# Kernel optimization log

Hardware: AMD Instinct MI355X
Metric: run time of the kernel (lower is better)

## Reference

```python
import jax, jax.numpy as jnp
import numpy as np

NUM_CUSTOMERS = 300000
NUM_PRODUCTS = 150000
NUM_GROUPS = 2000
NUM_BRANDS = 500
EMB_DIM = 64
NUM_LAYERS = 3


def setup_inputs() -> dict:
    key = jax.random.key(0)
    ks = jax.random.split(key, 20)
    def ri(k, n, hi):
        return jax.random.randint(k, (n,), 0, hi, dtype=jnp.int32)
    return {
        'cust_w': 0.1 * jax.random.normal(ks[0], (NUM_CUSTOMERS, EMB_DIM), jnp.float32),
        'prod_w': 0.1 * jax.random.normal(ks[1], (NUM_PRODUCTS, EMB_DIM), jnp.float32),
        'group_w': 0.1 * jax.random.normal(ks[2], (NUM_GROUPS, EMB_DIM), jnp.float32),
        'brand_w': 0.1 * jax.random.normal(ks[3], (NUM_BRANDS, EMB_DIM), jnp.float32),
        'purch_src': ri(ks[4], 2000000, NUM_CUSTOMERS),
        'purch_dst': ri(ks[5], 2000000, NUM_PRODUCTS),
        'pby_src': ri(ks[6], 2000000, NUM_PRODUCTS),
        'pby_dst': ri(ks[7], 2000000, NUM_CUSTOMERS),
        'sim_src': ri(ks[8], 500000, NUM_PRODUCTS),
        'sim_dst': ri(ks[9], 500000, NUM_PRODUCTS),
        'cop_src': ri(ks[10], 1000000, NUM_PRODUCTS),
        'cop_dst': ri(ks[11], 1000000, NUM_PRODUCTS),
        'bel_src': ri(ks[12], 150000, NUM_PRODUCTS),
        'bel_dst': ri(ks[13], 150000, NUM_GROUPS),
        'comp_src': ri(ks[14], 300000, NUM_PRODUCTS),
        'comp_dst': ri(ks[15], 300000, NUM_BRANDS),
    }


def _propagate(src_idx, tgt_idx, tgt_emb, n_src):
    # gather target embeddings along edges, scatter-add into source buckets,
    # normalize by source out-degree (clamped to >= 1) -- LightGCN mean-agg.
    msg = tgt_emb[tgt_idx]                                    # [E, D]
    agg = jax.ops.segment_sum(msg, src_idx, num_segments=n_src)
    cnt = jax.ops.segment_sum(jnp.ones(src_idx.shape, tgt_emb.dtype),
                              src_idx, num_segments=n_src)
    return agg / jnp.maximum(cnt, 1.0)[:, None]


def reference(cust_w, prod_w, group_w, brand_w,
              purch_src, purch_dst, pby_src, pby_dst,
              sim_src, sim_dst, cop_src, cop_dst,
              bel_src, bel_dst, comp_src, comp_dst):
    customer_emb, product_emb = cust_w, prod_w
    group_emb, brand_emb = group_w, brand_w
    customer_embs = [customer_emb]
    product_embs = [product_emb]
    for _ in range(NUM_LAYERS):
        customer_to_product = _propagate(purch_src, purch_dst, product_emb, NUM_CUSTOMERS)
        product_agg = product_emb
        product_agg = product_agg + _propagate(pby_src, pby_dst, customer_emb, NUM_PRODUCTS)
        product_agg = product_agg + 0.5 * _propagate(sim_src, sim_dst, product_emb, NUM_PRODUCTS)
        product_agg = product_agg + 0.3 * _propagate(cop_src, cop_dst, product_emb, NUM_PRODUCTS)
        product_agg = product_agg + 0.2 * _propagate(bel_src, bel_dst, group_emb, NUM_PRODUCTS)
        product_agg = product_agg + 0.2 * _propagate(comp_src, comp_dst, brand_emb, NUM_PRODUCTS)
        customer_emb = customer_to_product
        product_emb = product_agg
        customer_embs.append(customer_emb)
        product_embs.append(product_emb)
    final_customer = jnp.mean(jnp.stack(customer_embs, 0), axis=0)
    final_product = jnp.mean(jnp.stack(product_embs, 0), axis=0)
    # group/brand embeddings are never updated -> mean of identical copies
    return (final_customer, final_product, group_emb, brand_emb)
```

## Files before the change

### kernel.cpp

```cpp
#include <hip/hip_runtime.h>

#define NC 300000
#define NP 150000
#define NG 2000
#define NB 500
#define SCAN_B 1024
#define BK_SHIFT 11
#define BK_KEYS 2048
#define NBKT 513
#define CH 8192
#define ROWS (NP + NC)
#define RCH 4096

typedef unsigned int u32;
typedef float  f32x4 __attribute__((ext_vector_type(4)));
typedef unsigned int u32x4 __attribute__((ext_vector_type(4)));

static inline unsigned cdiv(long long a, long long b) { return (unsigned)((a + b - 1) / b); }

__device__ __forceinline__ float b2f(u32 h) {
    union { u32 u; float f; } c; c.u = h << 16; return c.f;
}
__device__ __forceinline__ u32 f2b(float f) {
    union { float f; u32 u; } c; c.f = f;
    return (c.u + 0x7FFFu + ((c.u >> 16) & 1u)) >> 16;
}
__device__ __forceinline__ void unpack8(uint4 v, float* o) {
    o[0] = b2f(v.x & 0xFFFFu); o[1] = b2f(v.x >> 16);
    o[2] = b2f(v.y & 0xFFFFu); o[3] = b2f(v.y >> 16);
    o[4] = b2f(v.z & 0xFFFFu); o[5] = b2f(v.z >> 16);
    o[6] = b2f(v.w & 0xFFFFu); o[7] = b2f(v.w >> 16);
}
__device__ __forceinline__ void unpack8v(u32x4 v, float* o) {
    o[0] = b2f(v.x & 0xFFFFu); o[1] = b2f(v.x >> 16);
    o[2] = b2f(v.y & 0xFFFFu); o[3] = b2f(v.y >> 16);
    o[4] = b2f(v.z & 0xFFFFu); o[5] = b2f(v.z >> 16);
    o[6] = b2f(v.w & 0xFFFFu); o[7] = b2f(v.w >> 16);
}
__device__ __forceinline__ uint4 pack8(const float* a) {
    uint4 v;
    v.x = f2b(a[0]) | (f2b(a[1]) << 16);
    v.y = f2b(a[2]) | (f2b(a[3]) << 16);
    v.z = f2b(a[4]) | (f2b(a[5]) << 16);
    v.w = f2b(a[6]) | (f2b(a[7]) << 16);
    return v;
}

__global__ void convert_all(const float* __restrict__ cw, const float* __restrict__ pw,
                            const float* __restrict__ gw, const float* __restrict__ bw,
                            uint4* __restrict__ c16, uint4* __restrict__ p16,
                            uint4* __restrict__ g16, uint4* __restrict__ b16,
                            float* __restrict__ outg, float* __restrict__ outb) {
    const int C8 = NC * 8, P8 = NP * 8, G8 = NG * 8, B8 = NB * 8;
    int i = blockIdx.x * blockDim.x + threadIdx.x;
    const float* in; uint4* out16; float* cpy = nullptr; int j;
    if (i < C8)                         { in = cw; out16 = c16; j = i; }
    else if ((j = i - C8) < P8)         { in = pw; out16 = p16; }
    else if ((j = i - C8 - P8) < G8)    { in = gw; out16 = g16; cpy = outg; }
    else if ((j = i - C8 - P8 - G8) < B8){ in = bw; out16 = b16; cpy = outb; }
    else return;
    const float4* p = (const float4*)(in + (size_t)j * 8);
    float4 a = p[0], b = p[1];
    float t[8] = { a.x, a.y, a.z, a.w, b.x, b.y, b.z, b.w };
    out16[j] = pack8(t);
    if (cpy) { float4* q = (float4*)(cpy + (size_t)j * 8); q[0] = a; q[1] = b; }
}

struct Edges6 {
    const int* src[6];
    const int* dst[6];
    int cum[7];
    int ctbase[7];
};

__global__ void bcount(Edges6 e, int* __restrict__ gcount, int total) {
    __shared__ int hist[NBKT];
    int t = threadIdx.x;
    int j0 = blockIdx.x * CH;
    for (int b = t; b < NBKT; b += blockDim.x) hist[b] = 0;
    __syncthreads();
    #pragma unroll 4
    for (int q = 0; q < CH / 256; ++q) {
        int j = j0 + q * 256 + t;
        if (j < total) {
            int k = 0;
            #pragma unroll
            for (int qq = 1; qq < 6; ++qq) k += (j >= e.cum[qq]);
            int key = e.ctbase[k] + __builtin_nontemporal_load(e.src[k] + (j - e.cum[k]));
            atomicAdd(&hist[key >> BK_SHIFT], 1);
        }
    }
    __syncthreads();
    for (int b = t; b < NBKT; b += blockDim.x) {
        int c = hist[b];
        if (c > 0) atomicAdd(gcount + b, c);
    }
}

__global__ void bscan(const int* __restrict__ gcount, int* __restrict__ gbase,
                      int* __restrict__ gcur, int nb) {
    __shared__ int sm[SCAN_B];
    int t = threadIdx.x;
    int v = (t < nb) ? gcount[t] : 0;
    sm[t] = v; __syncthreads();
    for (int off = 1; off < SCAN_B; off <<= 1) {
        int add = (t >= off) ? sm[t - off] : 0;
        __syncthreads();
        sm[t] += add; __syncthreads();
    }
    int excl = sm[t] - v;
    if (t < nb) { gbase[t] = excl; gcur[t] = excl; }
    if (t == nb - 1) gbase[nb] = sm[t];
}

__global__ void msplit(Edges6 e, int* __restrict__ gcur, u32* __restrict__ stage, int total) {
    __shared__ int hist[NBKT];
    __shared__ int bse[NBKT];
    int t = threadIdx.x;
    int j0 = blockIdx.x * CH;
    for (int b = t; b < NBKT; b += blockDim.x) hist[b] = 0;
    __syncthreads();
    #pragma unroll 4
    for (int q = 0; q < CH / 256; ++q) {
        int j = j0 + q * 256 + t;
        if (j < total) {
            int k = 0;
            #pragma unroll
            for (int qq = 1; qq < 6; ++qq) k += (j >= e.cum[qq]);
            int key = e.ctbase[k] + __builtin_nontemporal_load(e.src[k] + (j - e.cum[k]));
            atomicAdd(&hist[key >> BK_SHIFT], 1);
        }
    }
    __syncthreads();
    for (int b = t; b < NBKT; b += blockDim.x) {
        int c = hist[b];
        bse[b] = (c > 0) ? atomicAdd(gcur + b, c) : 0;
        hist[b] = 0;
    }
    __syncthreads();
    #pragma unroll 4
    for (int q = 0; q < CH / 256; ++q) {
        int j = j0 + q * 256 + t;
        if (j < total) {
            int k = 0;
            #pragma unroll
            for (int qq = 1; qq < 6; ++qq) k += (j >= e.cum[qq]);
            int jj = j - e.cum[k];
            int key = e.ctbase[k] + __builtin_nontemporal_load(e.src[k] + jj);
            int d = __builtin_nontemporal_load(e.dst[k] + jj);
            int b = key >> BK_SHIFT;
            int off = atomicAdd(&hist[b], 1);
            stage[bse[b] + off] = ((u32)(key & (BK_KEYS - 1)) << 19) | (u32)d;
        }
    }
}

__global__ void sortb(const int* __restrict__ gbase, const u32* __restrict__ stage,
                      int* __restrict__ pm, int* __restrict__ rp, int rtot) {
    __shared__ int cur[BK_KEYS];
    __shared__ int part[512];
    int b = blockIdx.x, t = threadIdx.x;
    int k0 = b << BK_SHIFT;
    int base = gbase[b], end = gbase[b + 1];
    for (int q = t; q < BK_KEYS; q += 512) cur[q] = 0;
    __syncthreads();
    for (int i = base + t; i < end; i += 512)
        atomicAdd(&cur[stage[i] >> 19], 1);
    __syncthreads();
    int a0 = cur[4 * t], a1 = cur[4 * t + 1], a2 = cur[4 * t + 2], a3 = cur[4 * t + 3];
    int s = a0 + a1 + a2 + a3;
    part[t] = s; __syncthreads();
    for (int off = 1; off < 512; off <<= 1) {
        int add = (t >= off) ? part[t - off] : 0;
        __syncthreads();
        part[t] += add; __syncthreads();
    }
    int c0 = base + part[t] - s;
    int c1 = c0 + a0, c2 = c1 + a1, c3 = c2 + a2;
    cur[4 * t] = c0; cur[4 * t + 1] = c1; cur[4 * t + 2] = c2; cur[4 * t + 3] = c3;
    int ki = k0 + 4 * t;
    if (ki + 3 < rtot) {
        *(int4*)(rp + ki) = make_int4(c0, c1, c2, c3);
    } else {
        if (ki     < rtot) rp[ki]     = c0;
        if (ki + 1 < rtot) rp[ki + 1] = c1;
        if (ki + 2 < rtot) rp[ki + 2] = c2;
        if (ki + 3 < rtot) rp[ki + 3] = c3;
    }
    __syncthreads();
    for (int i = base + t; i < end; i += 512) {
        u32 w = stage[i];
        int off = atomicAdd(&cur[w >> 19], 1);
        pm[off] = (int)(w & 0x7FFFFu);
    }
}

__device__ __forceinline__ int row_bin(const int* __restrict__ rp, int gid) {
    if (gid < NP) {
        int td = 0;
        #pragma unroll
        for (int k = 0; k < 5; ++k) {
            int o = (NC + 1) + k * (NP + 1) + gid;
            td += rp[o + 1] - rp[o];
        }
        return td < 127 ? td : 127;
    } else {
        int r = gid - NP;
        int d = rp[r + 1] - rp[r];
        return 128 + (d < 127 ? d : 127);
    }
}

__global__ void rowhist(const int* __restrict__ rp, int* __restrict__ gbinc, int rows) {
    __shared__ int hist[256];
    int t = threadIdx.x;
    hist[t] = 0;
    __syncthreads();
    int j0 = blockIdx.x * RCH;
    for (int q = 0; q < RCH / 256; ++q) {
        int j = j0 + q * 256 + t;
        if (j < rows) atomicAdd(&hist[row_bin(rp, j)], 1);
    }
    __syncthreads();
    int c = hist[t];
    if (c > 0) atomicAdd(gbinc + t, c);
}

__global__ void rowscan(const int* __restrict__ gbinc, int* __restrict__ gcur256) {
    __shared__ int sm[256];
    int t = threadIdx.x;
    int v = gbinc[t];
    sm[t] = v; __syncthreads();
    for (int off = 1; off < 256; off <<= 1) {
        int add = (t >= off) ? sm[t - off] : 0;
        __syncthreads();
        sm[t] += add; __syncthreads();
    }
    gcur256[t] = sm[t] - v;
}

__global__ void rowplace(const int* __restrict__ rp, int* __restrict__ gcur256,
                         int* __restrict__ perm, int rows) {
    __shared__ int hist[256];
    __shared__ int bse[256];
    int t = threadIdx.x;
    hist[t] = 0;
    __syncthreads();
    int j0 = blockIdx.x * RCH;
    for (int q = 0; q < RCH / 256; ++q) {
        int j = j0 + q * 256 + t;
        if (j < rows) atomicAdd(&hist[row_bin(rp, j)], 1);
    }
    __syncthreads();
    int c = hist[t];
    bse[t] = (c > 0) ? atomicAdd(gcur256 + t, c) : 0;
    hist[t] = 0;
    __syncthreads();
    for (int q = 0; q < RCH / 256; ++q) {
        int j = j0 + q * 256 + t;
        if (j < rows) {
            int b = row_bin(rp, j);
            int off = atomicAdd(&hist[b], 1);
            perm[bse[b] + off] = j;
        }
    }
}

__global__ void permrp(const int* __restrict__ rp, const int* __restrict__ perm,
                       int4* __restrict__ pA, int4* __restrict__ pB, int2* __restrict__ pC,
                       int2* __restrict__ cinfo, int rows) {
    int j = blockIdx.x * blockDim.x + threadIdx.x;
    if (j >= rows) return;
    int pg = perm[j];
    if (pg < NP) {
        const int* r0 = rp + (NC + 1) + pg;
        const int* r1 = r0 + (NP + 1);
        const int* r2 = r1 + (NP + 1);
        const int* r3 = r2 + (NP + 1);
        const int* r4 = r3 + (NP + 1);
        pA[j] = make_int4(r0[0], r0[1], r1[0], r1[1]);
        pB[j] = make_int4(r2[0], r2[1], r3[0], r3[1]);
        pC[j] = make_int2(r4[0], r4[1]);
    } else {
        int r = pg - NP;
        cinfo[j - NP] = make_int2(rp[r], rp[r + 1]);
    }
}

__device__ __forceinline__ void acc8(uint4 v, float* sum) {
    float t[8]; unpack8(v, t);
    #pragma unroll
    for (int k = 0; k < 8; ++k) sum[k] += t[k];
}
__device__ __forceinline__ void agg8se(int s, int e, const int* __restrict__ pm,
                                       const uint4* __restrict__ tgt,
                                       int lane, float w, float* acc) {
    float sum[8] = {0, 0, 0, 0, 0, 0, 0, 0};
    int i = s;
    for (; i + 4 <= e; i += 4) {
        int d0 = pm[i], d1 = pm[i + 1], d2 = pm[i + 2], d3 = pm[i + 3];
        uint4 v0 = tgt[(size_t)d0 * 8 + lane];
        uint4 v1 = tgt[(size_t)d1 * 8 + lane];
        uint4 v2 = tgt[(size_t)d2 * 8 + lane];
        uint4 v3 = tgt[(size_t)d3 * 8 + lane];
        acc8(v0, sum); acc8(v1, sum); acc8(v2, sum); acc8(v3, sum);
    }
    for (; i < e; ++i) {
        uint4 v = tgt[(size_t)pm[i] * 8 + lane];
        acc8(v, sum);
    }
    int deg = e - s;
    float sc = w / (float)(deg > 1 ? deg : 1);
    #pragma unroll
    for (int k = 0; k < 8; ++k) acc[k] += sum[k] * sc;
}

__global__ void layer_kernel(
    const int* __restrict__ perm,
    const int4* __restrict__ pA, const int4* __restrict__ pB, const int2* __restrict__ pC,
    const int2* __restrict__ cinfo,
    const int* __restrict__ pm,
    const uint4* __restrict__ c16, const uint4* __restrict__ p16,
    const uint4* __restrict__ g16, const uint4* __restrict__ b16,
    uint4* __restrict__ c16n, uint4* __restrict__ p16n,
    const float* __restrict__ cw, const float* __restrict__ pw,
    const uint4* __restrict__ s1c, const uint4* __restrict__ s1p,
    float* __restrict__ outc, float* __restrict__ outp,
    int mode)
{
    int t = blockIdx.x * blockDim.x + threadIdx.x;
    int gid = t >> 3;
    int lane = t & 7;
    float acc[8];
    if (gid < NP) {
        int row = perm[gid];
        size_t idx = (size_t)row * 8 + lane;
        int4 ia = pA[gid];
        int4 ib = pB[gid];
        int2 ic = pC[gid];
        float base[8]; unpack8(p16[idx], base);
        #pragma unroll
        for (int k = 0; k < 8; ++k) acc[k] = base[k];
        agg8se(ia.x, ia.y, pm, c16, lane, 1.0f, acc);
        agg8se(ia.z, ia.w, pm, p16, lane, 0.5f, acc);
        agg8se(ib.x, ib.y, pm, p16, lane, 0.3f, acc);
        agg8se(ib.z, ib.w, pm, g16, lane, 0.2f, acc);
        agg8se(ic.x, ic.y, pm, b16, lane, 0.2f, acc);
        if (mode != 2) {
            p16n[idx] = pack8(acc);
        } else {
            const f32x4* s0p = (const f32x4*)(pw + (size_t)row * 64 + lane * 8);
            f32x4 a0 = __builtin_nontemporal_load(s0p);
            f32x4 a1 = __builtin_nontemporal_load(s0p + 1);
            u32x4 s1v = __builtin_nontemporal_load((const u32x4*)&s1p[idx]);
            float sv[8]; unpack8v(s1v, sv);
            f32x4 o0, o1;
            o0.x = 0.25f * (a0.x + sv[0] + base[0] + acc[0]);
            o0.y = 0.25f * (a0.y + sv[1] + base[1] + acc[1]);
            o0.z = 0.25f * (a0.z + sv[2] + base[2] + acc[2]);
            o0.w = 0.25f * (a0.w + sv[3] + base[3] + acc[3]);
            o1.x = 0.25f * (a1.x + sv[4] + base[4] + acc[4]);
            o1.y = 0.25f * (a1.y + sv[5] + base[5] + acc[5]);
            o1.z = 0.25f * (a1.z + sv[6] + base[6] + acc[6]);
            o1.w = 0.25f * (a1.w + sv[7] + base[7] + acc[7]);
            f32x4* o = (f32x4*)(outp + (size_t)row * 64 + lane * 8);
            __builtin_nontemporal_store(o0, o);
            __builtin_nontemporal_store(o1, o + 1);
        }
    } else if (gid < ROWS) {
        int row = perm[gid] - NP;
        size_t idx = (size_t)row * 8 + lane;
        int2 se = cinfo[gid - NP];
        #pragma unroll
        for (int k = 0; k < 8; ++k) acc[k] = 0.f;
        agg8se(se.x, se.y, pm, p16, lane, 1.0f, acc);
        if (mode != 2) {
            c16n[idx] = pack8(acc);
        } else {
            float base[8]; unpack8(c16[idx], base);
            const f32x4* s0c = (const f32x4*)(cw + (size_t)row * 64 + lane * 8);
            f32x4 a0 = __builtin_nontemporal_load(s0c);
            f32x4 a1 = __builtin_nontemporal_load(s0c + 1);
            u32x4 s1v = __builtin_nontemporal_load((const u32x4*)&s1c[idx]);
            float sv[8]; unpack8v(s1v, sv);
            f32x4 o0, o1;
            o0.x = 0.25f * (a0.x + sv[0] + base[0] + acc[0]);
            o0.y = 0.25f * (a0.y + sv[1] + base[1] + acc[1]);
            o0.z = 0.25f * (a0.z + sv[2] + base[2] + acc[2]);
            o0.w = 0.25f * (a0.w + sv[3] + base[3] + acc[3]);
            o1.x = 0.25f * (a1.x + sv[4] + base[4] + acc[4]);
            o1.y = 0.25f * (a1.y + sv[5] + base[5] + acc[5]);
            o1.z = 0.25f * (a1.z + sv[6] + base[6] + acc[6]);
            o1.w = 0.25f * (a1.w + sv[7] + base[7] + acc[7]);
            f32x4* o = (f32x4*)(outc + (size_t)row * 64 + lane * 8);
            __builtin_nontemporal_store(o0, o);
            __builtin_nontemporal_store(o1, o + 1);
        }
    }
}

extern "C" void kernel_launch(void* const* d_in, const int* in_sizes, int n_in,
                              void* d_out, int out_size, void* d_ws, size_t ws_size,
                              hipStream_t stream) {
    const float* cust_w  = (const float*)d_in[0];
    const float* prod_w  = (const float*)d_in[1];
    const float* group_w = (const float*)d_in[2];
    const float* brand_w = (const float*)d_in[3];

    const int n_purch = in_sizes[4];
    const int n_pby   = in_sizes[6];
    const int n_sim   = in_sizes[8];
    const int n_cop   = in_sizes[10];
    const int n_bel   = in_sizes[12];
    const int n_comp  = in_sizes[14];
    const int n_edges[6] = { n_purch, n_pby, n_sim, n_cop, n_bel, n_comp };

    const size_t CSZ = (size_t)NC * 64;
    const size_t PSZ = (size_t)NP * 64;

    char* base = (char*)d_ws;
    uint4* c16A = (uint4*)base;                 base += (size_t)NC * 128;
    uint4* c16B = (uint4*)base;                 base += (size_t)NC * 128;
    uint4* p16A = (uint4*)base;                 base += (size_t)NP * 128;
    uint4* p16B = (uint4*)base;                 base += (size_t)NP * 128;
    uint4* g16  = (uint4*)base;                 base += (size_t)NG * 128;
    uint4* b16  = (uint4*)base;                 base += (size_t)NB * 128;

    const int RP_PURCH = NC + 1;
    const int RP_OTHER = NP + 1;
    const int RTOT = RP_PURCH + 5 * RP_OTHER;

    int* rp_all = (int*)base;                   base += (size_t)RTOT * 4;
    long long tot_edges = 0;
    for (int k = 0; k < 6; ++k) tot_edges += n_edges[k];
    int* pm_all = (int*)base;                   base += tot_edges * 4;
    u32* stage  = (u32*)base;                   base += tot_edges * 4;
    int* gcount = (int*)base;                   base += (size_t)NBKT * 4;
    int* gbase  = (int*)base;                   base += (size_t)(NBKT + 1) * 4;
    int* gcur   = (int*)base;                   base += (size_t)NBKT * 4;
    int* gbinc  = (int*)base;                   base += 256 * 4;
    int* gcur256= (int*)base;                   base += 256 * 4;
    int* perm   = (int*)base;                   base += (size_t)ROWS * 4;
    int4* pA    = (int4*)base;                  base += (size_t)NP * 16;
    int4* pB    = (int4*)base;                  base += (size_t)NP * 16;
    int2* pC    = (int2*)base;                  base += (size_t)NP * 8;
    int2* cinfo = (int2*)base;                  base += (size_t)NC * 8;

    float* out_c = (float*)d_out;
    float* out_p = out_c + CSZ;
    float* out_g = out_p + PSZ;
    float* out_b = out_g + (size_t)NG * 64;

    const int BT = 256;

    const long long CVT = (long long)(NC + NP + NG + NB) * 8;
    convert_all<<<cdiv(CVT, BT), BT, 0, stream>>>(
        cust_w, prod_w, group_w, brand_w, c16A, p16A, g16, b16, out_g, out_b);

    Edges6 E;
    E.src[0] = (const int*)d_in[4];  E.dst[0] = (const int*)d_in[5];
    E.src[1] = (const int*)d_in[6];  E.dst[1] = (const int*)d_in[7];
    E.src[2] = (const int*)d_in[8];  E.dst[2] = (const int*)d_in[9];
    E.src[3] = (const int*)d_in[10]; E.dst[3] = (const int*)d_in[11];
    E.src[4] = (const int*)d_in[12]; E.dst[4] = (const int*)d_in[13];
    E.src[5] = (const int*)d_in[14]; E.dst[5] = (const int*)d_in[15];
    E.cum[0] = 0;
    for (int k = 0; k < 6; ++k) E.cum[k + 1] = E.cum[k] + n_edges[k];
    E.ctbase[0] = 0;
    E.ctbase[1] = RP_PURCH;
    for (int k = 2; k < 6; ++k) E.ctbase[k] = E.ctbase[k - 1] + RP_OTHER;
    E.ctbase[6] = RTOT;
    const int TOT = E.cum[6];

    hipMemsetAsync(gcount, 0, (size_t)NBKT * 4, stream);
    hipMemsetAsync(gbinc, 0, 256 * 4, stream);
    bcount<<<cdiv(TOT, CH), BT, 0, stream>>>(E, gcount, TOT);
    bscan<<<1, SCAN_B, 0, stream>>>(gcount, gbase, gcur, NBKT);
    msplit<<<cdiv(TOT, CH), BT, 0, stream>>>(E, gcur, stage, TOT);
    sortb<<<NBKT, 512, 0, stream>>>(gbase, stage, pm_all, rp_all, RTOT);

    rowhist<<<cdiv(ROWS, RCH), 256, 0, stream>>>(rp_all, gbinc, ROWS);
    rowscan<<<1, 256, 0, stream>>>(gbinc, gcur256);
    rowplace<<<cdiv(ROWS, RCH), 256, 0, stream>>>(rp_all, gcur256, perm, ROWS);
    permrp<<<cdiv(ROWS, BT), BT, 0, stream>>>(rp_all, perm, pA, pB, pC, cinfo, ROWS);

    const long long LTHREADS = (long long)ROWS * 8;
    layer_kernel<<<cdiv(LTHREADS, BT), BT, 0, stream>>>(
        perm, pA, pB, pC, cinfo, pm_all,
        c16A, p16A, g16, b16, c16B, p16B,
        cust_w, prod_w, c16B, p16B, out_c, out_p, 0);
    layer_kernel<<<cdiv(LTHREADS, BT), BT, 0, stream>>>(
        perm, pA, pB, pC, cinfo, pm_all,
        c16B, p16B, g16, b16, c16A, p16A,
        cust_w, prod_w, c16B, p16B, out_c, out_p, 1);
    layer_kernel<<<cdiv(LTHREADS, BT), BT, 0, stream>>>(
        perm, pA, pB, pC, cinfo, pm_all,
        c16A, p16A, g16, b16, c16B, p16B,
        cust_w, prod_w, c16B, p16B,
        out_c, out_p, 2);
}
```

Before: 670.7 us.

## Interleave product relation CSR keys and merge five aggregation loops into one

Product-side edges are now keyed as src*5+relation, so each product's edges from all five relations sit contiguously in one CSR segment. The row-pointer array shrinks to one interleaved range, permrp writes 6 offsets instead of 10, and pB is removed. The layer kernel walks the whole product edge range in one unrolled-by-4 loop, choosing the source table and per-relation weight by comparing each index against the relation boundaries. This is meant to cut loop overhead and tail iterations for products with small per-relation degrees and to keep more gathers in flight, at the cost of extra per-edge selects.

```diff
diff --git a/kernel.cpp b/kernel.cpp
--- a/kernel.cpp
+++ b/kernel.cpp
@@ -7,6 +7,8 @@
 #define SCAN_B 1024
 #define BK_SHIFT 11
 #define BK_KEYS 2048
+#define CBASE (NC + 1)
+#define RTOT (CBASE + 5 * NP + 1)
 #define NBKT 513
 #define CH 8192
 #define ROWS (NP + NC)
@@ -70,8 +72,11 @@
     const int* src[6];
     const int* dst[6];
     int cum[7];
-    int ctbase[7];
 };
+
+__device__ __forceinline__ int edge_key(int k, int src) {
+    return (k == 0) ? src : CBASE + src * 5 + (k - 1);
+}
 
 __global__ void bcount(Edges6 e, int* __restrict__ gcount, int total) {
     __shared__ int hist[NBKT];
@@ -86,7 +91,7 @@
             int k = 0;
             #pragma unroll
             for (int qq = 1; qq < 6; ++qq) k += (j >= e.cum[qq]);
-            int key = e.ctbase[k] + __builtin_nontemporal_load(e.src[k] + (j - e.cum[k]));
+            int key = edge_key(k, __builtin_nontemporal_load(e.src[k] + (j - e.cum[k])));
             atomicAdd(&hist[key >> BK_SHIFT], 1);
         }
     }
@@ -127,7 +132,7 @@
             int k = 0;
             #pragma unroll
             for (int qq = 1; qq < 6; ++qq) k += (j >= e.cum[qq]);
-            int key = e.ctbase[k] + __builtin_nontemporal_load(e.src[k] + (j - e.cum[k]));
+            int key = edge_key(k, __builtin_nontemporal_load(e.src[k] + (j - e.cum[k])));
             atomicAdd(&hist[key >> BK_SHIFT], 1);
         }
     }
@@ -146,7 +151,7 @@
             #pragma unroll
             for (int qq = 1; qq < 6; ++qq) k += (j >= e.cum[qq]);
             int jj = j - e.cum[k];
-            int key = e.ctbase[k] + __builtin_nontemporal_load(e.src[k] + jj);
+            int key = edge_key(k, __builtin_nontemporal_load(e.src[k] + jj));
             int d = __builtin_nontemporal_load(e.dst[k] + jj);
             int b = key >> BK_SHIFT;
             int off = atomicAdd(&hist[b], 1);
@@ -197,12 +202,8 @@
 
 __device__ __forceinline__ int row_bin(const int* __restrict__ rp, int gid) {
     if (gid < NP) {
-        int td = 0;
-        #pragma unroll
-        for (int k = 0; k < 5; ++k) {
-            int o = (NC + 1) + k * (NP + 1) + gid;
-            td += rp[o + 1] - rp[o];
-        }
+        int o = CBASE + gid * 5;
+        int td = rp[o + 5] - rp[o];
         return td < 127 ? td : 127;
     } else {
         int r = gid - NP;
@@ -267,20 +268,15 @@
 }
 
 __global__ void permrp(const int* __restrict__ rp, const int* __restrict__ perm,
-                       int4* __restrict__ pA, int4* __restrict__ pB, int2* __restrict__ pC,
+                       int4* __restrict__ pA, int2* __restrict__ pC,
                        int2* __restrict__ cinfo, int rows) {
     int j = blockIdx.x * blockDim.x + threadIdx.x;
     if (j >= rows) return;
     int pg = perm[j];
     if (pg < NP) {
-        const int* r0 = rp + (NC + 1) + pg;
-        const int* r1 = r0 + (NP + 1);
-        const int* r2 = r1 + (NP + 1);
-        const int* r3 = r2 + (NP + 1);
-        const int* r4 = r3 + (NP + 1);
-        pA[j] = make_int4(r0[0], r0[1], r1[0], r1[1]);
-        pB[j] = make_int4(r2[0], r2[1], r3[0], r3[1]);
-        pC[j] = make_int2(r4[0], r4[1]);
+        const int* r0 = rp + CBASE + pg * 5;
+        pA[j] = make_int4(r0[0], r0[1], r0[2], r0[3]);
+        pC[j] = make_int2(r0[4], r0[5]);
     } else {
         int r = pg - NP;
         cinfo[j - NP] = make_int2(rp[r], rp[r + 1]);
@@ -294,7 +290,7 @@
 }
 __device__ __forceinline__ void agg8se(int s, int e, const int* __restrict__ pm,
                                        const uint4* __restrict__ tgt,
-                                       int lane, float w, float* acc) {
+                                       int lane, float* acc) {
     float sum[8] = {0, 0, 0, 0, 0, 0, 0, 0};
     int i = s;
     for (; i + 4 <= e; i += 4) {
@@ -310,14 +306,38 @@
         acc8(v, sum);
     }
     int deg = e - s;
-    float sc = w / (float)(deg > 1 ? deg : 1);
+    float sc = 1.0f / (float)(deg > 1 ? deg : 1);
     #pragma unroll
     for (int k = 0; k < 8; ++k) acc[k] += sum[k] * sc;
 }
 
+__device__ __forceinline__ const uint4* tblsel(int i, int b1, int b3, int b4,
+                                               const uint4* c16, const uint4* p16,
+                                               const uint4* g16, const uint4* b16) {
+    const uint4* t = c16;
+    if (i >= b1) t = p16;
+    if (i >= b3) t = g16;
+    if (i >= b4) t = b16;
+    return t;
+}
+__device__ __forceinline__ float sclsel(int i, int b1, int b2, int b3, int b4,
+                                        float s0, float s1, float s2, float s3, float s4) {
+    float s = s0;
+    if (i >= b1) s = s1;
+    if (i >= b2) s = s2;
+    if (i >= b3) s = s3;
+    if (i >= b4) s = s4;
+    return s;
+}
+__device__ __forceinline__ void accw(uint4 v, float s, float* acc) {
+    float t[8]; unpack8(v, t);
+    #pragma unroll
+    for (int k = 0; k < 8; ++k) acc[k] += t[k] * s;
+}
+
 __global__ void layer_kernel(
     const int* __restrict__ perm,
-    const int4* __restrict__ pA, const int4* __restrict__ pB, const int2* __restrict__ pC,
+    const int4* __restrict__ pA, const int2* __restrict__ pC,
     const int2* __restrict__ cinfo,
     const int* __restrict__ pm,
     const uint4* __restrict__ c16, const uint4* __restrict__ p16,
@@ -336,16 +356,41 @@
         int row = perm[gid];
         size_t idx = (size_t)row * 8 + lane;
         int4 ia = pA[gid];
-        int4 ib = pB[gid];
         int2 ic = pC[gid];
+        int b0 = ia.x, b1 = ia.y, b2 = ia.z, b3 = ia.w, b4 = ic.x, b5 = ic.y;
+        int d0g = b1 - b0, d1g = b2 - b1, d2g = b3 - b2, d3g = b4 - b3, d4g = b5 - b4;
+        float s0 = 1.0f / (float)(d0g > 1 ? d0g : 1);
+        float s1 = 0.5f / (float)(d1g > 1 ? d1g : 1);
+        float s2 = 0.3f / (float)(d2g > 1 ? d2g : 1);
+        float s3 = 0.2f / (float)(d3g > 1 ? d3g : 1);
+        float s4 = 0.2f / (float)(d4g > 1 ? d4g : 1);
         float base[8]; unpack8(p16[idx], base);
         #pragma unroll
         for (int k = 0; k < 8; ++k) acc[k] = base[k];
-        agg8se(ia.x, ia.y, pm, c16, lane, 1.0f, acc);
-        agg8se(ia.z, ia.w, pm, p16, lane, 0.5f, acc);
-        agg8se(ib.x, ib.y, pm, p16, lane, 0.3f, acc);
-        agg8se(ib.z, ib.w, pm, g16, lane, 0.2f, acc);
-        agg8se(ic.x, ic.y, pm, b16, lane, 0.2f, acc);
+        int i = b0;
+        for (; i + 4 <= b5; i += 4) {
+            int e0 = pm[i], e1 = pm[i + 1], e2 = pm[i + 2], e3 = pm[i + 3];
+            const uint4* t0 = tblsel(i,     b1, b3, b4, c16, p16, g16, b16);
+            const uint4* t1 = tblsel(i + 1, b1, b3, b4, c16, p16, g16, b16);
+            const uint4* t2 = tblsel(i + 2, b1, b3, b4, c16, p16, g16, b16);
+            const uint4* t3 = tblsel(i + 3, b1, b3, b4, c16, p16, g16, b16);
+            float w0 = sclsel(i,     b1, b2, b3, b4, s0, s1, s2, s3, s4);
+            float w1 = sclsel(i + 1, b1, b2, b3, b4, s0, s1, s2, s3, s4);
+            float w2 = sclsel(i + 2, b1, b2, b3, b4, s0, s1, s2, s3, s4);
+            float w3 = sclsel(i + 3, b1, b2, b3, b4, s0, s1, s2, s3, s4);
+            uint4 v0 = t0[(size_t)e0 * 8 + lane];
+            uint4 v1 = t1[(size_t)e1 * 8 + lane];
+            uint4 v2 = t2[(size_t)e2 * 8 + lane];
+            uint4 v3 = t3[(size_t)e3 * 8 + lane];
+            accw(v0, w0, acc); accw(v1, w1, acc); accw(v2, w2, acc); accw(v3, w3, acc);
+        }
+        for (; i < b5; ++i) {
+            int e0 = pm[i];
+            const uint4* t0 = tblsel(i, b1, b3, b4, c16, p16, g16, b16);
+            float w0 = sclsel(i, b1, b2, b3, b4, s0, s1, s2, s3, s4);
+            uint4 v0 = t0[(size_t)e0 * 8 + lane];
+            accw(v0, w0, acc);
+        }
         if (mode != 2) {
             p16n[idx] = pack8(acc);
         } else {
@@ -373,7 +418,7 @@
         int2 se = cinfo[gid - NP];
         #pragma unroll
         for (int k = 0; k < 8; ++k) acc[k] = 0.f;
-        agg8se(se.x, se.y, pm, p16, lane, 1.0f, acc);
+        agg8se(se.x, se.y, pm, p16, lane, acc);
         if (mode != 2) {
             c16n[idx] = pack8(acc);
         } else {
@@ -426,10 +471,6 @@
     uint4* g16  = (uint4*)base;                 base += (size_t)NG * 128;
     uint4* b16  = (uint4*)base;                 base += (size_t)NB * 128;
 
-    const int RP_PURCH = NC + 1;
-    const int RP_OTHER = NP + 1;
-    const int RTOT = RP_PURCH + 5 * RP_OTHER;
-
     int* rp_all = (int*)base;                   base += (size_t)RTOT * 4;
     long long tot_edges = 0;
     for (int k = 0; k < 6; ++k) tot_edges += n_edges[k];
@@ -442,7 +483,6 @@
     int* gcur256= (int*)base;                   base += 256 * 4;
     int* perm   = (int*)base;                   base += (size_t)ROWS * 4;
     int4* pA    = (int4*)base;                  base += (size_t)NP * 16;
-    int4* pB    = (int4*)base;                  base += (size_t)NP * 16;
     int2* pC    = (int2*)base;                  base += (size_t)NP * 8;
     int2* cinfo = (int2*)base;                  base += (size_t)NC * 8;
 
@@ -466,10 +506,6 @@
     E.src[5] = (const int*)d_in[14]; E.dst[5] = (const int*)d_in[15];
     E.cum[0] = 0;
     for (int k = 0; k < 6; ++k) E.cum[k + 1] = E.cum[k] + n_edges[k];
-    E.ctbase[0] = 0;
-    E.ctbase[1] = RP_PURCH;
-    for (int k = 2; k < 6; ++k) E.ctbase[k] = E.ctbase[k - 1] + RP_OTHER;
-    E.ctbase[6] = RTOT;
     const int TOT = E.cum[6];
 
     hipMemsetAsync(gcount, 0, (size_t)NBKT * 4, stream);
@@ -482,19 +518,19 @@
     rowhist<<<cdiv(ROWS, RCH), 256, 0, stream>>>(rp_all, gbinc, ROWS);
     rowscan<<<1, 256, 0, stream>>>(gbinc, gcur256);
     rowplace<<<cdiv(ROWS, RCH), 256, 0, stream>>>(rp_all, gcur256, perm, ROWS);
-    permrp<<<cdiv(ROWS, BT), BT, 0, stream>>>(rp_all, perm, pA, pB, pC, cinfo, ROWS);
+    permrp<<<cdiv(ROWS, BT), BT, 0, stream>>>(rp_all, perm, pA, pC, cinfo, ROWS);
 
     const long long LTHREADS = (long long)ROWS * 8;
     layer_kernel<<<cdiv(LTHREADS, BT), BT, 0, stream>>>(
-        perm, pA, pB, pC, cinfo, pm_all,
+        perm, pA, pC, cinfo, pm_all,
         c16A, p16A, g16, b16, c16B, p16B,
         cust_w, prod_w, c16B, p16B, out_c, out_p, 0);
     layer_kernel<<<cdiv(LTHREADS, BT), BT, 0, stream>>>(
-        perm, pA, pB, pC, cinfo, pm_all,
+        perm, pA, pC, cinfo, pm_all,
         c16B, p16B, g16, b16, c16A, p16A,
         cust_w, prod_w, c16B, p16B, out_c, out_p, 1);
     layer_kernel<<<cdiv(LTHREADS, BT), BT, 0, stream>>>(
-        perm, pA, pB, pC, cinfo, pm_all,
+        perm, pA, pC, cinfo, pm_all,
         c16A, p16A, g16, b16, c16B, p16B,
         cust_w, prod_w, c16B, p16B,
         out_c, out_p, 2);
```

Result: no change. 679.6 us (+1.3%).
